# Kernel optimization log

Measured on AMD Instinct MI355X. Metric: run time of the kernel, lower is better.

The kernel has to match this reference:

```python
import jax, jax.numpy as jnp
import numpy as np

# FNO 2D spectral conv: rfft2 -> keep 2 corner mode blocks -> complex einsum -> scatter -> irfft2
B, H, W, CIN, COUT = 8, 256, 256, 32, 32
M1, M2 = 16, 16
SCALE = 1.0 / (CIN * COUT)  # matches self.scale = 1/(in_channels*out_channels)


def setup_inputs() -> dict:
    key = jax.random.key(0)
    k1, k2, k3 = jax.random.split(key, 3)
    x = jax.random.normal(k1, (B, H, W, CIN), dtype=jnp.float32)  # channels_last input
    wshape = (2, CIN, COUT, M1, M2)  # (2**(ndims-1), in_c, out_c, m1, m2)
    w_real = (jax.random.uniform(k2, wshape, dtype=jnp.float32) * 2.0 - 1.0) * SCALE
    w_imag = (jax.random.uniform(k3, wshape, dtype=jnp.float32) * 2.0 - 1.0) * SCALE
    return {"x": x, "w_real": w_real, "w_imag": w_imag}


def reference(x, w_real, w_imag):
    w = jax.lax.complex(w_real, w_imag)  # complex64 spectral weights
    # channels_last -> channels_first: [B,H,W,C] -> [B,C,H,W]
    xc = jnp.transpose(x, (0, 3, 1, 2))
    x_ft = jnp.fft.rfft2(xc)  # [B, C, H, W//2+1] complex64
    # Two corner blocks along dim H (low and high freqs), low freqs along rfft dim.
    blocks = jnp.stack(
        [x_ft[:, :, :M1, :M2], x_ft[:, :, H - M1:, :M2]], axis=0
    )  # [2, B, Cin, M1, M2]
    # einsum 'wbi...,wio...->w...bo' (reordered here to wbohk; scatter layout equivalent)
    ob = jnp.einsum('wbihk,wiohk->wbohk', blocks, w)  # [2, B, Cout, M1, M2]
    out_ft = jnp.zeros((B, COUT, H, W // 2 + 1), dtype=ob.dtype)
    out_ft = out_ft.at[:, :, :M1, :M2].set(ob[0])
    out_ft = out_ft.at[:, :, H - M1:, :M2].set(ob[1])
    out = jnp.fft.irfft2(out_ft, s=(H, W))  # [B, Cout, H, W] float32
    # back to channels_last; activation is None (identity)
    return jnp.transpose(out, (0, 2, 3, 1))
```

## Files before the change

kernel.cpp:

```cpp
#include <hip/hip_runtime.h>
#include <math.h>


#define INV_HW (1.0f / 65536.0f)

__global__ void k_tw(float* __restrict__ E1, float* __restrict__ U,
                     float* __restrict__ E4) {
  int t = blockIdx.x * blockDim.x + threadIdx.x;
  const float step = 6.28318530717958647692f / 256.0f;
  if (t < 1024) {
    int w = t >> 3, kwp = t & 7;
    int me = (2 * kwp * w) & 255, mo = ((2 * kwp + 1) * w) & 255;
    float se, ce, so, co;
    sincosf(step * (float)me, &se, &ce);
    sincosf(step * (float)mo, &so, &co);
    ((float4*)E1)[t] = make_float4(ce, -se, co, -so);
  } else if (t < 1280) {
    int n = t - 1024;
    float s, c;
    sincosf(step * (float)n, &s, &c);
    ((float2*)U)[n] = make_float2(c, s);
  } else if (t < 2304) {
    int i = t - 1280;
    int w = i >> 3, q = i & 7;
    int me = (2 * q * w) & 255, mo = ((2 * q + 1) * w) & 255;
    float se, ce, so, co;
    sincosf(step * (float)me, &se, &ce);
    sincosf(step * (float)mo, &so, &co);
    float sc_e = (q == 0) ? INV_HW : 2.0f * INV_HW;
    float sc_o = 2.0f * INV_HW;
    ((float4*)E4)[i] = make_float4(sc_e * ce, sc_e * se, sc_o * co, sc_o * so);
  }
}

__global__ __launch_bounds__(256) void k_wdft(const float* __restrict__ x,
                                              const float* __restrict__ E1,
                                              float* __restrict__ T) {
  __shared__ __align__(16) float sxe[32 * 132];
  __shared__ __align__(16) float sxo[32 * 132];
  __shared__ float4 sE[1024];
  int bh = blockIdx.x, t = threadIdx.x;
  const float4* e1g = (const float4*)E1;
#pragma unroll
  for (int i = 0; i < 4; ++i) sE[t + 256 * i] = e1g[t + 256 * i];
  const float4* src = (const float4*)(x + (size_t)bh * 8192);
#pragma unroll
  for (int i = 0; i < 4; ++i) {
    int j = t + 256 * i;
    float4 a = src[j];
    float4 b = src[j + 1024];
    int w = j >> 3, c0 = (j & 7) * 4;
    sxe[(c0 + 0) * 132 + w] = a.x + b.x;
    sxe[(c0 + 1) * 132 + w] = a.y + b.y;
    sxe[(c0 + 2) * 132 + w] = a.z + b.z;
    sxe[(c0 + 3) * 132 + w] = a.w + b.w;
    sxo[(c0 + 0) * 132 + w] = a.x - b.x;
    sxo[(c0 + 1) * 132 + w] = a.y - b.y;
    sxo[(c0 + 2) * 132 + w] = a.z - b.z;
    sxo[(c0 + 3) * 132 + w] = a.w - b.w;
  }
  __syncthreads();
  int c = t >> 3, kwp = t & 7;
  const float* xe = sxe + c * 132;
  const float* xo = sxo + c * 132;
  const float4* eb = sE + kwp;
  float ar = 0, ai = 0, br = 0, bi = 0;
#pragma unroll 4
  for (int j = 0; j < 32; ++j) {
    float4 ye = *(const float4*)(xe + 4 * j);
    float4 yo = *(const float4*)(xo + 4 * j);
    float4 e0 = eb[(4 * j + 0) * 8];
    float4 e1 = eb[(4 * j + 1) * 8];
    float4 e2 = eb[(4 * j + 2) * 8];
    float4 e3 = eb[(4 * j + 3) * 8];
    ar += ye.x * e0.x; ai += ye.x * e0.y; br += yo.x * e0.z; bi += yo.x * e0.w;
    ar += ye.y * e1.x; ai += ye.y * e1.y; br += yo.y * e1.z; bi += yo.y * e1.w;
    ar += ye.z * e2.x; ai += ye.z * e2.y; br += yo.z * e2.z; bi += yo.z * e2.w;
    ar += ye.w * e3.x; ai += ye.w * e3.y; br += yo.w * e3.z; bi += yo.w * e3.w;
  }
  int b = bh >> 8, h = bh & 255;
  ((float4*)(T + ((size_t)(b * 32 + c) * 256 + h) * 32))[kwp] =
      make_float4(ar, ai, br, bi);
}

__global__ __launch_bounds__(1024) void k_hdft(const float* __restrict__ T,
                                               const float* __restrict__ U,
                                               float* __restrict__ X) {
  __shared__ __align__(16) float sT[8192];
  __shared__ float2 sU[256];
  __shared__ float4 sRed[768];
  int t = threadIdx.x;
  const float4* src = (const float4*)(T + (size_t)blockIdx.x * 8192);
  float4* dT = (float4*)sT;
  dT[t] = src[t];
  dT[t + 1024] = src[t + 1024];
  if (t < 256) sU[t] = ((const float2*)U)[t];
  __syncthreads();
  int kw = t & 15, kh = (t >> 4) & 15, s = t >> 8;
  float sg = (kh & 1) ? -1.f : 1.f;
  int st1 = kh, st2 = (kh + 240) & 255;
  int h0 = s * 32;
  int ph1 = (st1 * h0) & 255;
  int ph2 = (st2 * h0) & 255;
  float x0r = 0, x0i = 0, x1r = 0, x1i = 0;
#pragma unroll 4
  for (int hh = 0; hh < 32; ++hh) {
    int h = h0 + hh;
    float2 t0 = *(const float2*)(sT + h * 32 + kw * 2);
    float2 t1 = *(const float2*)(sT + (h + 128) * 32 + kw * 2);
    float tpx = fmaf(sg, t1.x, t0.x);
    float tpy = fmaf(sg, t1.y, t0.y);
    float2 e1 = sU[ph1];
    float2 e2 = sU[ph2];
    x0r += tpx * e1.x + tpy * e1.y;
    x0i += tpy * e1.x - tpx * e1.y;
    x1r += tpx * e2.x + tpy * e2.y;
    x1i += tpy * e2.x - tpx * e2.y;
    ph1 = (ph1 + st1) & 255;
    ph2 = (ph2 + st2) & 255;
  }
  if (s > 0) sRed[(s - 1) * 256 + (t & 255)] = make_float4(x0r, x0i, x1r, x1i);
  __syncthreads();
  if (s == 0) {
#pragma unroll
    for (int k = 0; k < 3; ++k) {
      float4 p = sRed[k * 256 + t];
      x0r += p.x; x0i += p.y; x1r += p.z; x1i += p.w;
    }
    float2* Xb = (float2*)(X + (size_t)blockIdx.x * 1024);
    Xb[kh * 16 + kw] = make_float2(x0r, x0i);
    Xb[(kh + 16) * 16 + kw] = make_float2(x1r, x1i);
  }
}

__global__ __launch_bounds__(512) void k_mixidft(const float* __restrict__ X,
                                                 const float* __restrict__ wr,
                                                 const float* __restrict__ wi,
                                                 const float* __restrict__ U,
                                                 float* __restrict__ G) {
  __shared__ __align__(16) float2 sY[512];
  __shared__ float2 sU[256];
  int b = blockIdx.x >> 5, o = blockIdx.x & 31;
  int t = threadIdx.x;
  if (t < 256) sU[t] = ((const float2*)U)[t];
  {
    int kw = t & 15, row = t >> 4;
    int blk = row >> 4, khl = row & 15;
    const float* wr0 =
        wr + (size_t)blk * 262144 + (size_t)o * 256 + khl * 16 + kw;
    const float* wi0 =
        wi + (size_t)blk * 262144 + (size_t)o * 256 + khl * 16 + kw;
    const float* Xb = X + (size_t)b * 32768 + row * 32 + kw * 2;
    float yr = 0, yi = 0;
#pragma unroll 4
    for (int i = 0; i < 32; ++i) {
      float2 xv = *(const float2*)(Xb + i * 1024);
      float a = wr0[i * 8192], bb = wi0[i * 8192];
      yr += xv.x * a - xv.y * bb;
      yi += xv.x * bb + xv.y * a;
    }
    sY[row * 16 + kw] = make_float2(yr, yi);
  }
  __syncthreads();
  const float4* sY4 = (const float4*)sY;
  int q = t & 7, hr = t >> 3;
#pragma unroll
  for (int hb = 0; hb < 2; ++hb) {
    int h = hr + hb * 64;
    float se0r = 0, se0i = 0, se1r = 0, se1i = 0;
    float so0r = 0, so0i = 0, so1r = 0, so1i = 0;
#pragma unroll 4
    for (int kh2 = 0; kh2 < 16; ++kh2) {
      int khe = 2 * kh2, kho = khe + 1;
      int khae = khe < 16 ? khe : khe + 224;
      int khao = kho < 16 ? kho : kho + 224;
      float2 ee = sU[(khae * h) & 255];
      float2 eo = sU[(khao * h) & 255];
      float4 yE = sY4[khe * 8 + q];
      float4 yO = sY4[kho * 8 + q];
      se0r += yE.x * ee.x - yE.y * ee.y;
      se0i += yE.x * ee.y + yE.y * ee.x;
      se1r += yE.z * ee.x - yE.w * ee.y;
      se1i += yE.z * ee.y + yE.w * ee.x;
      so0r += yO.x * eo.x - yO.y * eo.y;
      so0i += yO.x * eo.y + yO.y * eo.x;
      so1r += yO.z * eo.x - yO.w * eo.y;
      so1i += yO.z * eo.y + yO.w * eo.x;
    }
    float* g0 = G + (((size_t)b * 256 + h) * 32 + o) * 32 + 4 * q;
    float* g1 = G + (((size_t)b * 256 + h + 128) * 32 + o) * 32 + 4 * q;
    *(float4*)g0 =
        make_float4(se0r + so0r, se0i + so0i, se1r + so1r, se1i + so1i);
    *(float4*)g1 =
        make_float4(se0r - so0r, se0i - so0i, se1r - so1r, se1i - so1i);
  }
}

__global__ __launch_bounds__(256) void k_widft(const float* __restrict__ G,
                                               const float* __restrict__ E4,
                                               float* __restrict__ out) {
  __shared__ float sG[32 * 33];
  __shared__ float4 sE4[1024];
  int bh = blockIdx.x, t = threadIdx.x;
  const float4* e4g = (const float4*)E4;
#pragma unroll
  for (int i = 0; i < 4; ++i) sE4[t + 256 * i] = e4g[t + 256 * i];
  {
    float4 v = ((const float4*)(G + (size_t)bh * 1024))[t];
    int o = t >> 3, p = t & 7;
    float* d = sG + o * 33 + p * 4;
    d[0] = v.x; d[1] = v.y; d[2] = v.z; d[3] = v.w;
  }
  __syncthreads();
  int o = t & 31, wb = t >> 5;
  float g[32];
#pragma unroll
  for (int k = 0; k < 32; ++k) g[k] = sG[o * 33 + k];
  float* ob = out + (size_t)bh * 8192 + o;
#pragma unroll 2
  for (int j = 0; j < 16; ++j) {
    int w = wb * 16 + j;
    float se = 0.f, so = 0.f;
#pragma unroll
    for (int q = 0; q < 8; ++q) {
      float4 e = sE4[w * 8 + q];
      se += g[4 * q] * e.x - g[4 * q + 1] * e.y;
      so += g[4 * q + 2] * e.z - g[4 * q + 3] * e.w;
    }
    ob[(size_t)w * 32] = se + so;
    ob[(size_t)(w + 128) * 32] = se - so;
  }
}

extern "C" void kernel_launch(void* const* d_in, const int* in_sizes, int n_in,
                              void* d_out, int out_size, void* d_ws,
                              size_t ws_size, hipStream_t stream) {
  const float* x = (const float*)d_in[0];
  const float* wr = (const float*)d_in[1];
  const float* wi = (const float*)d_in[2];
  float* out = (float*)d_out;
  float* ws = (float*)d_ws;

  float* E1 = ws;
  float* U  = ws + 4096;
  float* E4 = ws + 4608;
  float* T  = ws + 8704;
  float* X  = ws + 2105856;
  float* G  = T;

  k_tw<<<9, 256, 0, stream>>>(E1, U, E4);
  k_wdft<<<2048, 256, 0, stream>>>(x, E1, T);
  k_hdft<<<256, 1024, 0, stream>>>(T, U, X);
  k_mixidft<<<256, 512, 0, stream>>>(X, wr, wi, U, G);
  k_widft<<<2048, 256, 0, stream>>>(G, E4, out);
}
```

Before: 157.8 us.

## Drop twiddle kernel, compute twiddles in-kernel, halve W-DFT twiddle table

Removes the separate twiddle-generation launch. Each kernel now computes its own cos/sin tables with sincosf directly into shared memory. The W-direction DFT processes two rows per 512-thread block and uses a half-size twiddle table, splitting each sum into low and high halves combined with a parity sign. This removes one launch and the global twiddle traffic, at the cost of redundant sincosf work in every block.

```diff
diff --git a/kernel.cpp b/kernel.cpp
--- a/kernel.cpp
+++ b/kernel.cpp
@@ -3,88 +3,93 @@
 
 
 #define INV_HW (1.0f / 65536.0f)
-
-__global__ void k_tw(float* __restrict__ E1, float* __restrict__ U,
-                     float* __restrict__ E4) {
-  int t = blockIdx.x * blockDim.x + threadIdx.x;
-  const float step = 6.28318530717958647692f / 256.0f;
-  if (t < 1024) {
+#define STEP256 (6.28318530717958647692f / 256.0f)
+
+__global__ __launch_bounds__(512) void k_wdft(const float* __restrict__ x,
+                                              float* __restrict__ T) {
+  __shared__ __align__(16) float sxe[2][32 * 136];
+  __shared__ __align__(16) float sxo[2][32 * 136];
+  __shared__ __align__(16) float4 sE[512];
+  int t = threadIdx.x;
+  int b = blockIdx.x >> 7, h0 = (blockIdx.x & 127) << 1;
+  int sub = t >> 8, tsub = t & 255;
+  const float4* src =
+      (const float4*)(x + ((size_t)(b * 256 + h0 + sub)) * 8192);
+  float4 av[4], bv[4];
+#pragma unroll
+  for (int i = 0; i < 4; ++i) {
+    av[i] = src[tsub + 256 * i];
+    bv[i] = src[tsub + 256 * i + 1024];
+  }
+  {
     int w = t >> 3, kwp = t & 7;
     int me = (2 * kwp * w) & 255, mo = ((2 * kwp + 1) * w) & 255;
     float se, ce, so, co;
-    sincosf(step * (float)me, &se, &ce);
-    sincosf(step * (float)mo, &so, &co);
-    ((float4*)E1)[t] = make_float4(ce, -se, co, -so);
-  } else if (t < 1280) {
-    int n = t - 1024;
-    float s, c;
-    sincosf(step * (float)n, &s, &c);
-    ((float2*)U)[n] = make_float2(c, s);
-  } else if (t < 2304) {
-    int i = t - 1280;
-    int w = i >> 3, q = i & 7;
-    int me = (2 * q * w) & 255, mo = ((2 * q + 1) * w) & 255;
-    float se, ce, so, co;
-    sincosf(step * (float)me, &se, &ce);
-    sincosf(step * (float)mo, &so, &co);
-    float sc_e = (q == 0) ? INV_HW : 2.0f * INV_HW;
-    float sc_o = 2.0f * INV_HW;
-    ((float4*)E4)[i] = make_float4(sc_e * ce, sc_e * se, sc_o * co, sc_o * so);
-  }
-}
-
-__global__ __launch_bounds__(256) void k_wdft(const float* __restrict__ x,
-                                              const float* __restrict__ E1,
-                                              float* __restrict__ T) {
-  __shared__ __align__(16) float sxe[32 * 132];
-  __shared__ __align__(16) float sxo[32 * 132];
-  __shared__ float4 sE[1024];
-  int bh = blockIdx.x, t = threadIdx.x;
-  const float4* e1g = (const float4*)E1;
-#pragma unroll
-  for (int i = 0; i < 4; ++i) sE[t + 256 * i] = e1g[t + 256 * i];
-  const float4* src = (const float4*)(x + (size_t)bh * 8192);
+    sincosf(STEP256 * (float)me, &se, &ce);
+    sincosf(STEP256 * (float)mo, &so, &co);
+    sE[t] = make_float4(ce, -se, co, -so);
+  }
+  float* pe = &sxe[sub][0];
+  float* po = &sxo[sub][0];
 #pragma unroll
   for (int i = 0; i < 4; ++i) {
-    int j = t + 256 * i;
-    float4 a = src[j];
-    float4 b = src[j + 1024];
+    int j = tsub + 256 * i;
     int w = j >> 3, c0 = (j & 7) * 4;
-    sxe[(c0 + 0) * 132 + w] = a.x + b.x;
-    sxe[(c0 + 1) * 132 + w] = a.y + b.y;
-    sxe[(c0 + 2) * 132 + w] = a.z + b.z;
-    sxe[(c0 + 3) * 132 + w] = a.w + b.w;
-    sxo[(c0 + 0) * 132 + w] = a.x - b.x;
-    sxo[(c0 + 1) * 132 + w] = a.y - b.y;
-    sxo[(c0 + 2) * 132 + w] = a.z - b.z;
-    sxo[(c0 + 3) * 132 + w] = a.w - b.w;
-  }
-  __syncthreads();
-  int c = t >> 3, kwp = t & 7;
-  const float* xe = sxe + c * 132;
-  const float* xo = sxo + c * 132;
+    float4 a = av[i], bb = bv[i];
+    pe[(c0 + 0) * 136 + w] = a.x + bb.x;
+    pe[(c0 + 1) * 136 + w] = a.y + bb.y;
+    pe[(c0 + 2) * 136 + w] = a.z + bb.z;
+    pe[(c0 + 3) * 136 + w] = a.w + bb.w;
+    po[(c0 + 0) * 136 + w] = a.x - bb.x;
+    po[(c0 + 1) * 136 + w] = a.y - bb.y;
+    po[(c0 + 2) * 136 + w] = a.z - bb.z;
+    po[(c0 + 3) * 136 + w] = a.w - bb.w;
+  }
+  __syncthreads();
+  int c = (t >> 3) & 31, kwp = t & 7;
+  const float* xe = pe + c * 136;
+  const float* xo = po + c * 136;
   const float4* eb = sE + kwp;
-  float ar = 0, ai = 0, br = 0, bi = 0;
-#pragma unroll 4
-  for (int j = 0; j < 32; ++j) {
-    float4 ye = *(const float4*)(xe + 4 * j);
-    float4 yo = *(const float4*)(xo + 4 * j);
+  float arl = 0, ail = 0, brl = 0, bil = 0;
+  float arh = 0, aih = 0, brh = 0, bih = 0;
+#pragma unroll 4
+  for (int j = 0; j < 16; ++j) {
+    float4 yel = *(const float4*)(xe + 4 * j);
+    float4 yeh = *(const float4*)(xe + 64 + 4 * j);
+    float4 yol = *(const float4*)(xo + 4 * j);
+    float4 yoh = *(const float4*)(xo + 64 + 4 * j);
     float4 e0 = eb[(4 * j + 0) * 8];
     float4 e1 = eb[(4 * j + 1) * 8];
     float4 e2 = eb[(4 * j + 2) * 8];
     float4 e3 = eb[(4 * j + 3) * 8];
-    ar += ye.x * e0.x; ai += ye.x * e0.y; br += yo.x * e0.z; bi += yo.x * e0.w;
-    ar += ye.y * e1.x; ai += ye.y * e1.y; br += yo.y * e1.z; bi += yo.y * e1.w;
-    ar += ye.z * e2.x; ai += ye.z * e2.y; br += yo.z * e2.z; bi += yo.z * e2.w;
-    ar += ye.w * e3.x; ai += ye.w * e3.y; br += yo.w * e3.z; bi += yo.w * e3.w;
-  }
-  int b = bh >> 8, h = bh & 255;
+    arl += yel.x * e0.x; ail += yel.x * e0.y;
+    brl += yol.x * e0.z; bil += yol.x * e0.w;
+    arh += yeh.x * e0.x; aih += yeh.x * e0.y;
+    brh += yoh.x * e0.z; bih += yoh.x * e0.w;
+    arl += yel.y * e1.x; ail += yel.y * e1.y;
+    brl += yol.y * e1.z; bil += yol.y * e1.w;
+    arh += yeh.y * e1.x; aih += yeh.y * e1.y;
+    brh += yoh.y * e1.z; bih += yoh.y * e1.w;
+    arl += yel.z * e2.x; ail += yel.z * e2.y;
+    brl += yol.z * e2.z; bil += yol.z * e2.w;
+    arh += yeh.z * e2.x; aih += yeh.z * e2.y;
+    brh += yoh.z * e2.z; bih += yoh.z * e2.w;
+    arl += yel.w * e3.x; ail += yel.w * e3.y;
+    brl += yol.w * e3.z; bil += yol.w * e3.w;
+    arh += yeh.w * e3.x; aih += yeh.w * e3.y;
+    brh += yoh.w * e3.z; bih += yoh.w * e3.w;
+  }
+  float sgn = (kwp & 1) ? -1.f : 1.f;
+  float ar = fmaf(sgn, arh, arl);
+  float ai = fmaf(sgn, aih, ail);
+  float br = fmaf(sgn, bih, brl);
+  float bi = fmaf(-sgn, brh, bil);
+  int h = h0 + sub;
   ((float4*)(T + ((size_t)(b * 32 + c) * 256 + h) * 32))[kwp] =
       make_float4(ar, ai, br, bi);
 }
 
 __global__ __launch_bounds__(1024) void k_hdft(const float* __restrict__ T,
-                                               const float* __restrict__ U,
                                                float* __restrict__ X) {
   __shared__ __align__(16) float sT[8192];
   __shared__ float2 sU[256];
@@ -94,7 +99,11 @@
   float4* dT = (float4*)sT;
   dT[t] = src[t];
   dT[t + 1024] = src[t + 1024];
-  if (t < 256) sU[t] = ((const float2*)U)[t];
+  if (t < 256) {
+    float s, c;
+    sincosf(STEP256 * (float)t, &s, &c);
+    sU[t] = make_float2(c, s);
+  }
   __syncthreads();
   int kw = t & 15, kh = (t >> 4) & 15, s = t >> 8;
   float sg = (kh & 1) ? -1.f : 1.f;
@@ -136,13 +145,16 @@
 __global__ __launch_bounds__(512) void k_mixidft(const float* __restrict__ X,
                                                  const float* __restrict__ wr,
                                                  const float* __restrict__ wi,
-                                                 const float* __restrict__ U,
                                                  float* __restrict__ G) {
   __shared__ __align__(16) float2 sY[512];
   __shared__ float2 sU[256];
   int b = blockIdx.x >> 5, o = blockIdx.x & 31;
   int t = threadIdx.x;
-  if (t < 256) sU[t] = ((const float2*)U)[t];
+  if (t < 256) {
+    float s, c;
+    sincosf(STEP256 * (float)t, &s, &c);
+    sU[t] = make_float2(c, s);
+  }
   {
     int kw = t & 15, row = t >> 4;
     int blk = row >> 4, khl = row & 15;
@@ -197,16 +209,24 @@
 }
 
 __global__ __launch_bounds__(256) void k_widft(const float* __restrict__ G,
-                                               const float* __restrict__ E4,
                                                float* __restrict__ out) {
   __shared__ float sG[32 * 33];
-  __shared__ float4 sE4[1024];
+  __shared__ __align__(16) float4 sE4[1024];
   int bh = blockIdx.x, t = threadIdx.x;
-  const float4* e4g = (const float4*)E4;
-#pragma unroll
-  for (int i = 0; i < 4; ++i) sE4[t + 256 * i] = e4g[t + 256 * i];
+  float4 v = ((const float4*)(G + (size_t)bh * 1024))[t];
+#pragma unroll
+  for (int r = 0; r < 4; ++r) {
+    int i = t + 256 * r;
+    int w = i >> 3, q = i & 7;
+    int me = (2 * q * w) & 255, mo = ((2 * q + 1) * w) & 255;
+    float se, ce, so, co;
+    sincosf(STEP256 * (float)me, &se, &ce);
+    sincosf(STEP256 * (float)mo, &so, &co);
+    float sc_e = (q == 0) ? INV_HW : 2.0f * INV_HW;
+    sE4[i] = make_float4(sc_e * ce, sc_e * se, 2.0f * INV_HW * co,
+                         2.0f * INV_HW * so);
+  }
   {
-    float4 v = ((const float4*)(G + (size_t)bh * 1024))[t];
     int o = t >> 3, p = t & 7;
     float* d = sG + o * 33 + p * 4;
     d[0] = v.x; d[1] = v.y; d[2] = v.z; d[3] = v.w;
@@ -241,16 +261,12 @@
   float* out = (float*)d_out;
   float* ws = (float*)d_ws;
 
-  float* E1 = ws;
-  float* U  = ws + 4096;
-  float* E4 = ws + 4608;
-  float* T  = ws + 8704;
-  float* X  = ws + 2105856;
-  float* G  = T;
-
-  k_tw<<<9, 256, 0, stream>>>(E1, U, E4);
-  k_wdft<<<2048, 256, 0, stream>>>(x, E1, T);
-  k_hdft<<<256, 1024, 0, stream>>>(T, U, X);
-  k_mixidft<<<256, 512, 0, stream>>>(X, wr, wi, U, G);
-  k_widft<<<2048, 256, 0, stream>>>(G, E4, out);
-}
+  float* T = ws;
+  float* X = ws + 2097152;
+  float* G = T;
+
+  k_wdft<<<1024, 512, 0, stream>>>(x, T);
+  k_hdft<<<256, 1024, 0, stream>>>(T, X);
+  k_mixidft<<<256, 512, 0, stream>>>(X, wr, wi, G);
+  k_widft<<<2048, 256, 0, stream>>>(G, out);
+}
```

New measurement: 156.2 us. Within noise of the previous version (-1.0%).
